# Performance work log

Measured on AMD Instinct MI355X. Metric: run time of the kernel, lower is better.

The kernel has to match this reference:

```python
import jax, jax.numpy as jnp
import numpy as np

B, N, C = 2, 20000, 128
E = 320000
H, COUT = 4, 64
HD = 256  # hidden_dim == H*COUT -> projection is None
ED = 16
L = 3  # LSTM layers


def setup_inputs() -> dict:
    key = jax.random.key(0)
    ks = jax.random.split(key, 16)
    return {
        "x": jax.random.normal(ks[0], (B, N, C), jnp.float32),
        "edge_index": jax.random.randint(ks[1], (2, E), 0, N),
        "edge_attr": jax.random.normal(ks[2], (E, ED), jnp.float32),
        "lin_w": jax.random.normal(ks[3], (C, H * COUT), jnp.float32) / np.sqrt(C),
        "att_src": jax.random.normal(ks[4], (1, H, COUT), jnp.float32) * 0.1,
        "att_dst": jax.random.normal(ks[5], (1, H, COUT), jnp.float32) * 0.1,
        "lin_edge_w": jax.random.normal(ks[6], (ED, H * COUT), jnp.float32) / np.sqrt(ED),
        "att_edge": jax.random.normal(ks[7], (1, H, COUT), jnp.float32) * 0.1,
        "gat_bias": jnp.zeros((H * COUT,), jnp.float32),
        "w_ih": jax.random.normal(ks[8], (L, 4 * HD, HD), jnp.float32) / np.sqrt(HD),
        "w_hh": jax.random.normal(ks[9], (L, 4 * HD, HD), jnp.float32) / np.sqrt(HD),
        "b_ih": jnp.zeros((L, 4 * HD), jnp.float32),
        "b_hh": jnp.zeros((L, 4 * HD), jnp.float32),
        "ln_g": jnp.ones((HD,), jnp.float32),
        "ln_b": jnp.zeros((HD,), jnp.float32),
    }


def reference(x, edge_index, edge_attr, lin_w, att_src, att_dst, lin_edge_w,
              att_edge, gat_bias, w_ih, w_hh, b_ih, b_hh, ln_g, ln_b):
    Bn = B * N
    # ---- GAT: linear transform ----
    xt = (x.reshape(Bn, C) @ lin_w).reshape(Bn, H, COUT)
    # batch-offset edge index, then append self-loops for every node
    off = (jnp.arange(B, dtype=edge_index.dtype) * N)[:, None]
    src = (edge_index[0][None, :] + off).reshape(-1)
    dst = (edge_index[1][None, :] + off).reshape(-1)
    loop = jnp.arange(Bn, dtype=edge_index.dtype)
    src = jnp.concatenate([src, loop])  # [Etot] = [B*E + B*N]
    dst = jnp.concatenate([dst, loop])
    # edge features: shared 2D edge_attr is repeated per batch, zeros on self-loops
    ea = (edge_attr @ lin_edge_w).reshape(E, H, COUT)
    ea = jnp.concatenate([jnp.tile(ea, (B, 1, 1)),
                          jnp.zeros((Bn, H, COUT), xt.dtype)], axis=0)
    # ---- message: gather, score, segment-softmax ----
    x_j = xt[src]  # [Etot, H, COUT]
    x_i = xt[dst]
    alpha = ((x_j * att_src).sum(-1) + (x_i * att_dst).sum(-1)
             + (ea * att_edge).sum(-1))  # [Etot, H]
    alpha = jax.nn.leaky_relu(alpha, 0.2)
    m = jax.ops.segment_max(alpha, dst, num_segments=Bn)
    alpha = jnp.exp(alpha - m[dst])
    s = jax.ops.segment_sum(alpha, dst, num_segments=Bn)
    alpha = alpha / (s[dst] + 1e-16)  # PyG softmax eps; dropout inactive (eval)
    # ---- aggregate (scatter-add) ----
    out = jax.ops.segment_sum(x_j * alpha[..., None], dst, num_segments=Bn)
    spatial = out.reshape(Bn, H * COUT) + gat_bias  # concat heads, [Bn, HD]
    # ---- 3-layer LSTM, seq_len=1, zero initial state (h_prev=None) ----
    h_in = spatial
    hs, cs = [], []
    for l in range(L):
        # h0 = c0 = 0 -> w_hh contributes nothing; inter-layer dropout inactive
        gates = h_in @ w_ih[l].T + b_ih[l] + b_hh[l]
        i, f, g, o = jnp.split(gates, 4, axis=-1)  # PyTorch gate order i,f,g,o
        c = jax.nn.sigmoid(i) * jnp.tanh(g)
        h = jax.nn.sigmoid(o) * jnp.tanh(c)
        hs.append(h)
        cs.append(c)
        h_in = h
    # ---- LayerNorm ----
    h_out = h_in.reshape(B, N, HD)
    mu = h_out.mean(-1, keepdims=True)
    var = ((h_out - mu) ** 2).mean(-1, keepdims=True)
    h_out = (h_out - mu) / jnp.sqrt(var + 1e-5) * ln_g + ln_b
    return h_out, jnp.stack(hs), jnp.stack(cs)
```

## Files before the change

### kernel.cpp

```cpp
#include <hip/hip_runtime.h>
#include <stdint.h>

#define NB_    20000
#define CB_    128
#define EE_    320000
#define BN_    40000
#define BE_    640000
#define ETOT_  680000

typedef __attribute__((ext_vector_type(4))) float f4;
typedef __attribute__((ext_vector_type(4))) unsigned short us4;
typedef __attribute__((ext_vector_type(4))) unsigned int ui4;
typedef __attribute__((ext_vector_type(8))) __bf16 bf16x8;

static __device__ __forceinline__ unsigned short f2bf(float f){
    union { float f; unsigned int u; } v; v.f = f;
    unsigned int u = v.u;
    u += 0x7FFFu + ((u >> 16) & 1u);
    return (unsigned short)(u >> 16);
}
static __device__ __forceinline__ float bf2f(unsigned short b){
    union { unsigned int u; float f; } v; v.u = ((unsigned int)b) << 16;
    return v.f;
}
static __device__ __forceinline__ float sigf(float x){ return 1.f/(1.f+__expf(-x)); }
static __device__ __forceinline__ float tanhfast(float x){ return 2.f/(1.f+__expf(-2.f*x)) - 1.f; }
static __device__ __forceinline__ f4 fmax4(f4 a, f4 b){
    f4 r; r[0]=fmaxf(a[0],b[0]); r[1]=fmaxf(a[1],b[1]); r[2]=fmaxf(a[2],b[2]); r[3]=fmaxf(a[3],b[3]); return r;
}
static __device__ __forceinline__ void gl_lds16(const void* g, void* l){
    __builtin_amdgcn_global_load_lds((const __attribute__((address_space(1))) void*)g,
                                     (__attribute__((address_space(3))) void*)l, 16, 0, 0);
}

__global__ void w2_kernel(const float* __restrict__ lew, const float* __restrict__ ae,
                          float* __restrict__ W2){
    int t = threadIdx.x;
    int d = t >> 2, h = t & 3;
    float s = 0.f;
    for (int c = 0; c < 64; ++c) s += lew[d*256 + h*64 + c] * ae[h*64 + c];
    W2[d*4 + h] = s;
}

__global__ void pack_linwT_kernel(const float* __restrict__ lw, unsigned short* __restrict__ wt){
    int tid = blockIdx.x*256 + threadIdx.x;
    int n = tid >> 7, k = tid & 127;
    wt[n*128 + k] = f2bf(lw[k*256 + n]);
}

__global__ void pack_lstmw_kernel(const float* __restrict__ w_ih, unsigned short* __restrict__ Bp){
    int tid = blockIdx.x*256 + threadIdx.x;
    int l   = tid / 196608;
    int rem = tid - l*196608;
    int p = rem >> 8, k = rem & 255;
    int jb = p / 192, q2 = p - jb*192;
    int chunk = q2 / 48, r = q2 - chunk*48;
    int gate = r >> 4, jj = r & 15;
    int gor = (gate == 0) ? 0 : (gate == 1 ? 2 : 3);
    int srcrow = gor*256 + jb*64 + chunk*16 + jj;
    Bp[tid] = f2bf(w_ih[(l*1024 + srcrow)*256 + k]);
}

__global__ void pack_bias_kernel(const float* __restrict__ b_ih, const float* __restrict__ b_hh,
                                 float* __restrict__ bp){
    int tid = blockIdx.x*256 + threadIdx.x;
    if (tid >= 2304) return;
    int l = tid / 768, p = tid - l*768;
    int jb = p / 192, q2 = p - jb*192;
    int chunk = q2 / 48, r = q2 - chunk*48;
    int gate = r >> 4, jj = r & 15;
    int gor = (gate == 0) ? 0 : (gate == 1 ? 2 : 3);
    int srcrow = gor*256 + jb*64 + chunk*16 + jj;
    bp[tid] = b_ih[l*1024 + srcrow] + b_hh[l*1024 + srcrow];
}

__global__ __launch_bounds__(256) void gemm1_kernel(const float* __restrict__ x,
        const unsigned short* __restrict__ wt, unsigned short* __restrict__ xt){
    __shared__ unsigned short As[64*72];
    __shared__ unsigned short Bs[64*72];
    const int tid = threadIdx.x;
    const int bm = blockIdx.x, bn = blockIdx.y;
    const int lane = tid & 63, w = tid >> 6;
    const int wm = w & 1, wn = w >> 1;
    const int nl = lane & 15, q = lane >> 4;
    f4 acc[2][2] = {};
    for (int kc = 0; kc < 128; kc += 64) {
        #pragma unroll
        for (int it = 0; it < 4; ++it) {
            int s = tid + it*256;
            int row = s >> 4, c4 = s & 15;
            f4 v = *(const f4*)&x[(bm*64+row)*128 + kc + c4*4];
            us4 o; o[0]=f2bf(v[0]); o[1]=f2bf(v[1]); o[2]=f2bf(v[2]); o[3]=f2bf(v[3]);
            *(us4*)&As[row*72 + c4*4] = o;
        }
        #pragma unroll
        for (int it = 0; it < 2; ++it) {
            int s = tid + it*256;
            int row = s >> 3, c = s & 7;
            *(ui4*)&Bs[row*72 + c*8] = *(const ui4*)&wt[(bn*64+row)*128 + kc + c*8];
        }
        __syncthreads();
        #pragma unroll
        for (int kk = 0; kk < 64; kk += 32) {
            bf16x8 a[2], b[2];
            #pragma unroll
            for (int mt = 0; mt < 2; ++mt) a[mt] = *(const bf16x8*)&As[(wm*32 + mt*16 + nl)*72 + kk + q*8];
            #pragma unroll
            for (int nt = 0; nt < 2; ++nt) b[nt] = *(const bf16x8*)&Bs[(wn*32 + nt*16 + nl)*72 + kk + q*8];
            #pragma unroll
            for (int mt = 0; mt < 2; ++mt)
                #pragma unroll
                for (int nt = 0; nt < 2; ++nt)
                    acc[mt][nt] = __builtin_amdgcn_mfma_f32_16x16x32_bf16(a[mt], b[nt], acc[mt][nt], 0, 0, 0);
        }
        __syncthreads();
    }
    #pragma unroll
    for (int mt = 0; mt < 2; ++mt)
        #pragma unroll
        for (int nt = 0; nt < 2; ++nt)
            #pragma unroll
            for (int r = 0; r < 4; ++r) {
                int row = bm*64 + wm*32 + mt*16 + q*4 + r;
                int col = bn*64 + wn*32 + nt*16 + nl;
                xt[row*256 + col] = f2bf(acc[mt][nt][r]);
            }
}

__global__ __launch_bounds__(256) void scores_kernel(const unsigned short* __restrict__ xt,
        const float* __restrict__ att_src, const float* __restrict__ att_dst,
        float* __restrict__ s_src, float* __restrict__ s_dst){
    int n = blockIdx.x*4 + (threadIdx.x >> 6);
    int lane = threadIdx.x & 63;
    us4 xv = *(const us4*)&xt[n*256 + lane*4];
    f4 as = *(const f4*)&att_src[lane*4];
    f4 ad = *(const f4*)&att_dst[lane*4];
    float x0=bf2f(xv[0]), x1=bf2f(xv[1]), x2=bf2f(xv[2]), x3=bf2f(xv[3]);
    float ps = x0*as[0]+x1*as[1]+x2*as[2]+x3*as[3];
    float pd = x0*ad[0]+x1*ad[1]+x2*ad[2]+x3*ad[3];
    #pragma unroll
    for (int o = 1; o < 16; o <<= 1) { ps += __shfl_xor(ps, o, 64); pd += __shfl_xor(pd, o, 64); }
    if ((lane & 15) == 0) {
        s_src[n*4 + (lane>>4)] = ps;
        s_dst[n*4 + (lane>>4)] = pd;
    }
}

__global__ __launch_bounds__(256) void eascore_kernel(const float* __restrict__ ea,
        const float* __restrict__ W2, float* __restrict__ esc){
    __shared__ float w2s[64];
    if (threadIdx.x < 64) w2s[threadIdx.x] = W2[threadIdx.x];
    __syncthreads();
    int e = blockIdx.x*256 + threadIdx.x;
    if (e >= EE_) return;
    f4 acc = {};
    #pragma unroll
    for (int d = 0; d < 16; ++d) {
        float v = ea[e*16 + d];
        f4 wv = *(const f4*)&w2s[d*4];
        acc += v * wv;
    }
    *(f4*)&esc[e*4] = acc;
}

__global__ __launch_bounds__(256) void deghist_kernel(const int* __restrict__ ei, int* __restrict__ deg){
    int e = blockIdx.x*256 + threadIdx.x;
    if (e >= ETOT_) return;
    int dst;
    if (e < BE_) { int b = e / EE_, ee = e - b*EE_; dst = ei[EE_ + ee] + b*NB_; }
    else dst = e - BE_;
    atomicAdd(&deg[dst], 1);
}

__global__ __launch_bounds__(256) void scan1_kernel(const int* __restrict__ deg,
        int* __restrict__ inc, int* __restrict__ bsum){
    __shared__ int sd[256];
    int t = threadIdx.x, i = blockIdx.x*256 + t;
    int v = (i < BN_) ? deg[i] : 0;
    sd[t] = v; __syncthreads();
    #pragma unroll
    for (int d = 1; d < 256; d <<= 1) {
        int x = (t >= d) ? sd[t-d] : 0; __syncthreads();
        sd[t] += x; __syncthreads();
    }
    inc[i] = sd[t];
    if (t == 255) bsum[blockIdx.x] = sd[255];
}

__global__ __launch_bounds__(256) void scan2_kernel(const int* __restrict__ bsum,
        int* __restrict__ bpre, int nb){
    __shared__ int sd[256];
    int t = threadIdx.x;
    int v = (t < nb) ? bsum[t] : 0;
    sd[t] = v; __syncthreads();
    #pragma unroll
    for (int d = 1; d < 256; d <<= 1) {
        int x = (t >= d) ? sd[t-d] : 0; __syncthreads();
        sd[t] += x; __syncthreads();
    }
    if (t < nb) bpre[t] = sd[t] - v;
}

__global__ __launch_bounds__(256) void scan3_kernel(const int* __restrict__ inc,
        const int* __restrict__ deg, const int* __restrict__ bpre,
        int* __restrict__ offs, int* __restrict__ cur){
    int i = blockIdx.x*256 + threadIdx.x;
    if (i >= BN_) return;
    int o = inc[i] - deg[i] + bpre[blockIdx.x];
    offs[i] = o; cur[i] = o;
}

__global__ __launch_bounds__(256) void scatter_kernel(const int* __restrict__ ei,
        const float* __restrict__ s_src, const float* __restrict__ s_dst,
        const float* __restrict__ esc, int* __restrict__ cur,
        int* __restrict__ csr_src, float* __restrict__ csr_alpha){
    int e = blockIdx.x*256 + threadIdx.x;
    if (e >= ETOT_) return;
    int src, dst; f4 a;
    if (e < BE_) {
        int b = e / EE_, ee = e - b*EE_;
        src = ei[ee] + b*NB_;
        dst = ei[EE_ + ee] + b*NB_;
        a = *(const f4*)&esc[ee*4];
    } else {
        src = dst = e - BE_;
        a = (f4){0.f, 0.f, 0.f, 0.f};
    }
    a += *(const f4*)&s_src[src*4];
    a += *(const f4*)&s_dst[dst*4];
    #pragma unroll
    for (int h = 0; h < 4; ++h) a[h] = (a[h] > 0.f) ? a[h] : 0.2f*a[h];
    int pos = atomicAdd(&cur[dst], 1);
    csr_src[pos] = src;
    *(f4*)&csr_alpha[pos*4] = a;
}

__global__ __launch_bounds__(256) void aggregate_kernel(const int* __restrict__ offs,
        const int* __restrict__ deg, const int* __restrict__ csr_src,
        const float* __restrict__ csr_alpha, const unsigned short* __restrict__ xt,
        const float* __restrict__ gat_bias, unsigned short* __restrict__ spat){
    int n = blockIdx.x*4 + (threadIdx.x >> 6);
    int lane = threadIdx.x & 63;
    int start = offs[n], d = deg[n];
    f4 mv = {-1e30f, -1e30f, -1e30f, -1e30f};
    for (int i = lane; i < d; i += 64)
        mv = fmax4(mv, *(const f4*)&csr_alpha[(start+i)*4]);
    #pragma unroll
    for (int o = 1; o < 64; o <<= 1) {
        f4 t; t[0]=__shfl_xor(mv[0],o,64); t[1]=__shfl_xor(mv[1],o,64);
        t[2]=__shfl_xor(mv[2],o,64); t[3]=__shfl_xor(mv[3],o,64);
        mv = fmax4(mv, t);
    }
    f4 sv = {};
    for (int i = lane; i < d; i += 64) {
        f4 a = *(const f4*)&csr_alpha[(start+i)*4];
        sv[0] += __expf(a[0]-mv[0]); sv[1] += __expf(a[1]-mv[1]);
        sv[2] += __expf(a[2]-mv[2]); sv[3] += __expf(a[3]-mv[3]);
    }
    #pragma unroll
    for (int o = 1; o < 64; o <<= 1) {
        sv[0]+=__shfl_xor(sv[0],o,64); sv[1]+=__shfl_xor(sv[1],o,64);
        sv[2]+=__shfl_xor(sv[2],o,64); sv[3]+=__shfl_xor(sv[3],o,64);
    }
    int h = lane >> 4;
    float mh = (h==0)?mv[0]:(h==1)?mv[1]:(h==2)?mv[2]:mv[3];
    float sh = (h==0)?sv[0]:(h==1)?sv[1]:(h==2)?sv[2]:sv[3];
    f4 accv = {};
    for (int base = 0; base < d; base += 64) {
        int cnt = min(64, d - base);
        int srcl = (base + lane < d) ? csr_src[start+base+lane] : 0;
        for (int i = 0; i < cnt; ++i) {
            int srcn = __shfl(srcl, i, 64);
            float av = csr_alpha[(start+base+i)*4 + h];
            float ew = __expf(av - mh);
            us4 xv = *(const us4*)&xt[srcn*256 + lane*4];
            accv[0] += ew * bf2f(xv[0]);
            accv[1] += ew * bf2f(xv[1]);
            accv[2] += ew * bf2f(xv[2]);
            accv[3] += ew * bf2f(xv[3]);
        }
    }
    float invs = 1.f / (sh + 1e-16f);
    f4 gb = *(const f4*)&gat_bias[lane*4];
    accv = accv * invs + gb;
    us4 o4; o4[0]=f2bf(accv[0]); o4[1]=f2bf(accv[1]); o4[2]=f2bf(accv[2]); o4[3]=f2bf(accv[3]);
    *(us4*)&spat[n*256 + lane*4] = o4;
}

__global__ __launch_bounds__(256) void lstm_kernel(const unsigned short* __restrict__ A,
        const unsigned short* __restrict__ Bp, const float* __restrict__ bias,
        float* __restrict__ hs_out, float* __restrict__ cs_out, unsigned short* __restrict__ hnext){
    __shared__ unsigned short As[64*64];
    __shared__ unsigned short Bs[192*64];
    const int tid = threadIdx.x;
    const int bm = blockIdx.x, jb = blockIdx.y;
    const int lane = tid & 63, w = tid >> 6;
    const int nl = lane & 15, q = lane >> 4;
    const int rsub = lane >> 3, csub = lane & 7;
    const int swz = ((csub ^ rsub) << 4);
    f4 acc[4][3] = {};
    const char* Ab = (const char*)A + ((size_t)(bm*64 + rsub))*512 + swz;
    const char* Bb = (const char*)(Bp + (size_t)jb*192*256) + (size_t)rsub*512 + swz;
    for (int kc = 0; kc < 256; kc += 64) {
        #pragma unroll
        for (int i = 0; i < 2; ++i) {
            int t = 2*w + i;
            gl_lds16(Ab + (size_t)t*4096 + kc*2, (char*)As + t*1024);
        }
        #pragma unroll
        for (int i = 0; i < 6; ++i) {
            int t = 6*w + i;
            gl_lds16(Bb + (size_t)t*4096 + kc*2, (char*)Bs + t*1024);
        }
        __syncthreads();
        #pragma unroll
        for (int kk = 0; kk < 64; kk += 32) {
            const int cswz = (kk*2 + q*16) ^ ((nl & 7) << 4);
            bf16x8 a[4], b[3];
            #pragma unroll
            for (int mt = 0; mt < 4; ++mt)
                a[mt] = *(const bf16x8*)((const char*)As + (mt*16 + nl)*128 + cswz);
            #pragma unroll
            for (int gt = 0; gt < 3; ++gt)
                b[gt] = *(const bf16x8*)((const char*)Bs + (w*48 + gt*16 + nl)*128 + cswz);
            #pragma unroll
            for (int mt = 0; mt < 4; ++mt)
                #pragma unroll
                for (int gt = 0; gt < 3; ++gt)
                    acc[mt][gt] = __builtin_amdgcn_mfma_f32_16x16x32_bf16(a[mt], b[gt], acc[mt][gt], 0, 0, 0);
        }
        __syncthreads();
    }
    const int j = jb*64 + w*16 + nl;
    const float bi = bias[jb*192 + w*48 +  0 + nl];
    const float bg = bias[jb*192 + w*48 + 16 + nl];
    const float bo = bias[jb*192 + w*48 + 32 + nl];
    #pragma unroll
    for (int mt = 0; mt < 4; ++mt)
        #pragma unroll
        for (int r = 0; r < 4; ++r) {
            int m = bm*64 + mt*16 + q*4 + r;
            float iv = acc[mt][0][r] + bi;
            float gv = acc[mt][1][r] + bg;
            float ov = acc[mt][2][r] + bo;
            float c = sigf(iv) * tanhfast(gv);
            float hh = sigf(ov) * tanhfast(c);
            cs_out[m*256 + j] = c;
            hs_out[m*256 + j] = hh;
            if (hnext) hnext[m*256 + j] = f2bf(hh);
        }
}

__global__ __launch_bounds__(256) void ln_kernel(const float* __restrict__ hin,
        const float* __restrict__ g, const float* __restrict__ b, float* __restrict__ out){
    int n = blockIdx.x*4 + (threadIdx.x >> 6);
    int lane = threadIdx.x & 63;
    f4 v = *(const f4*)&hin[n*256 + lane*4];
    float s = v[0]+v[1]+v[2]+v[3];
    float ss = v[0]*v[0]+v[1]*v[1]+v[2]*v[2]+v[3]*v[3];
    #pragma unroll
    for (int o = 1; o < 64; o <<= 1) { s += __shfl_xor(s,o,64); ss += __shfl_xor(ss,o,64); }
    float mu = s * (1.f/256.f);
    float var = ss * (1.f/256.f) - mu*mu;
    float rstd = rsqrtf(var + 1e-5f);
    f4 gg = *(const f4*)&g[lane*4], bb = *(const f4*)&b[lane*4];
    f4 o4 = (v - mu) * rstd * gg + bb;
    *(f4*)&out[n*256 + lane*4] = o4;
}

static inline char* carve(char*& p, size_t bytes){
    char* r = p; p += (bytes + 255) & ~(size_t)255; return r;
}

extern "C" void kernel_launch(void* const* d_in, const int* in_sizes, int n_in,
                              void* d_out, int out_size, void* d_ws, size_t ws_size,
                              hipStream_t stream){
    const float* x         = (const float*)d_in[0];
    const int*   ei        = (const int*)  d_in[1];
    const float* edge_attr = (const float*)d_in[2];
    const float* lin_w     = (const float*)d_in[3];
    const float* att_src   = (const float*)d_in[4];
    const float* att_dst   = (const float*)d_in[5];
    const float* lin_edge_w= (const float*)d_in[6];
    const float* att_edge  = (const float*)d_in[7];
    const float* gat_bias  = (const float*)d_in[8];
    const float* w_ih      = (const float*)d_in[9];
    const float* b_ih      = (const float*)d_in[11];
    const float* b_hh      = (const float*)d_in[12];
    const float* ln_g      = (const float*)d_in[13];
    const float* ln_b      = (const float*)d_in[14];

    float* out = (float*)d_out;
    float* hs_base = out + 10240000;
    float* cs_base = out + 40960000;

    unsigned short* xt   = (unsigned short*)(out + 0);
    float* esc           = out + 10240000;
    int*   csr_src       = (int*)(out + 40960000);
    float* csr_alpha     = out + 41640000;
    unsigned short* spat = (unsigned short*)(out + 51200000);
    unsigned short* h0   = (unsigned short*)(out + 61440000);
    unsigned short* h1   = (unsigned short*)(out + 0);

    char* p = (char*)d_ws;
    float* W2          = (float*)carve(p, 64*4);
    float* s_src       = (float*)carve(p, (size_t)BN_*4*4);
    float* s_dst       = (float*)carve(p, (size_t)BN_*4*4);
    unsigned short* lwT= (unsigned short*)carve(p, 32768*2);
    unsigned short* Bp = (unsigned short*)carve(p, 589824*2);
    float* biasP       = (float*)carve(p, 2304*4);
    int* deg           = (int*)carve(p, BN_*4);
    int* inc           = (int*)carve(p, 157*256*4);
    int* bsum          = (int*)carve(p, 256*4);
    int* bpre          = (int*)carve(p, 256*4);
    int* offs          = (int*)carve(p, BN_*4);
    int* cur           = (int*)carve(p, BN_*4);

    hipMemsetAsync(deg, 0, BN_*4, stream);
    w2_kernel<<<1, 64, 0, stream>>>(lin_edge_w, att_edge, W2);
    pack_linwT_kernel<<<128, 256, 0, stream>>>(lin_w, lwT);
    pack_lstmw_kernel<<<2304, 256, 0, stream>>>(w_ih, Bp);
    pack_bias_kernel<<<9, 256, 0, stream>>>(b_ih, b_hh, biasP);

    gemm1_kernel<<<dim3(625, 4), 256, 0, stream>>>(x, lwT, xt);
    scores_kernel<<<10000, 256, 0, stream>>>(xt, att_src, att_dst, s_src, s_dst);
    eascore_kernel<<<1250, 256, 0, stream>>>(edge_attr, W2, esc);

    deghist_kernel<<<2657, 256, 0, stream>>>(ei, deg);
    scan1_kernel<<<157, 256, 0, stream>>>(deg, inc, bsum);
    scan2_kernel<<<1, 256, 0, stream>>>(bsum, bpre, 157);
    scan3_kernel<<<157, 256, 0, stream>>>(inc, deg, bpre, offs, cur);
    scatter_kernel<<<2657, 256, 0, stream>>>(ei, s_src, s_dst, esc, cur, csr_src, csr_alpha);
    aggregate_kernel<<<10000, 256, 0, stream>>>(offs, deg, csr_src, csr_alpha, xt, gat_bias, spat);

    lstm_kernel<<<dim3(625, 4), 256, 0, stream>>>(spat, Bp,          biasP,        hs_base,            cs_base,            h0);
    lstm_kernel<<<dim3(625, 4), 256, 0, stream>>>(h0,   Bp + 196608, biasP + 768,  hs_base + 10240000, cs_base + 10240000, h1);
    lstm_kernel<<<dim3(625, 4), 256, 0, stream>>>(h1,   Bp + 393216, biasP + 1536, hs_base + 20480000, cs_base + 20480000, (unsigned short*)nullptr);

    ln_kernel<<<10000, 256, 0, stream>>>(hs_base + 20480000, ln_g, ln_b, out);
}
```

Measured before the change: 600.2 us.

## Merge prep kernels, drop softmax max pass, keep LSTM weights in registers

Folds the four weight-packing launches into one prep kernel to cut launch overhead. The aggregate kernel drops its max and sum pre-passes and instead exponentiates the raw scores while accumulating the normaliser in the same loop. This removes two passes over the edge scores but gives up max subtraction, so large scores could overflow. The LSTM GEMM loads the whole 64x256 A tile into LDS once and keeps each wave's B slice in registers, with launch bounds asking for two blocks per CU. This removes the per-k-chunk barriers but raises register pressure.

```diff
diff --git a/kernel.cpp b/kernel.cpp
--- a/kernel.cpp
+++ b/kernel.cpp
@@ -25,53 +25,51 @@
 }
 static __device__ __forceinline__ float sigf(float x){ return 1.f/(1.f+__expf(-x)); }
 static __device__ __forceinline__ float tanhfast(float x){ return 2.f/(1.f+__expf(-2.f*x)) - 1.f; }
-static __device__ __forceinline__ f4 fmax4(f4 a, f4 b){
-    f4 r; r[0]=fmaxf(a[0],b[0]); r[1]=fmaxf(a[1],b[1]); r[2]=fmaxf(a[2],b[2]); r[3]=fmaxf(a[3],b[3]); return r;
-}
 static __device__ __forceinline__ void gl_lds16(const void* g, void* l){
     __builtin_amdgcn_global_load_lds((const __attribute__((address_space(1))) void*)g,
                                      (__attribute__((address_space(3))) void*)l, 16, 0, 0);
 }
 
-__global__ void w2_kernel(const float* __restrict__ lew, const float* __restrict__ ae,
-                          float* __restrict__ W2){
-    int t = threadIdx.x;
-    int d = t >> 2, h = t & 3;
-    float s = 0.f;
-    for (int c = 0; c < 64; ++c) s += lew[d*256 + h*64 + c] * ae[h*64 + c];
-    W2[d*4 + h] = s;
-}
-
-__global__ void pack_linwT_kernel(const float* __restrict__ lw, unsigned short* __restrict__ wt){
-    int tid = blockIdx.x*256 + threadIdx.x;
-    int n = tid >> 7, k = tid & 127;
-    wt[n*128 + k] = f2bf(lw[k*256 + n]);
-}
-
-__global__ void pack_lstmw_kernel(const float* __restrict__ w_ih, unsigned short* __restrict__ Bp){
-    int tid = blockIdx.x*256 + threadIdx.x;
-    int l   = tid / 196608;
-    int rem = tid - l*196608;
-    int p = rem >> 8, k = rem & 255;
-    int jb = p / 192, q2 = p - jb*192;
-    int chunk = q2 / 48, r = q2 - chunk*48;
-    int gate = r >> 4, jj = r & 15;
-    int gor = (gate == 0) ? 0 : (gate == 1 ? 2 : 3);
-    int srcrow = gor*256 + jb*64 + chunk*16 + jj;
-    Bp[tid] = f2bf(w_ih[(l*1024 + srcrow)*256 + k]);
-}
-
-__global__ void pack_bias_kernel(const float* __restrict__ b_ih, const float* __restrict__ b_hh,
-                                 float* __restrict__ bp){
-    int tid = blockIdx.x*256 + threadIdx.x;
-    if (tid >= 2304) return;
-    int l = tid / 768, p = tid - l*768;
-    int jb = p / 192, q2 = p - jb*192;
-    int chunk = q2 / 48, r = q2 - chunk*48;
-    int gate = r >> 4, jj = r & 15;
-    int gor = (gate == 0) ? 0 : (gate == 1 ? 2 : 3);
-    int srcrow = gor*256 + jb*64 + chunk*16 + jj;
-    bp[tid] = b_ih[l*1024 + srcrow] + b_hh[l*1024 + srcrow];
+__global__ __launch_bounds__(256) void prep_kernel(const float* __restrict__ lew,
+        const float* __restrict__ ae, float* __restrict__ W2,
+        const float* __restrict__ lw, unsigned short* __restrict__ wt,
+        const float* __restrict__ w_ih, unsigned short* __restrict__ Bp,
+        const float* __restrict__ b_ih, const float* __restrict__ b_hh,
+        float* __restrict__ bp){
+    int bi = blockIdx.x, t = threadIdx.x;
+    if (bi == 0) {
+        if (t < 64) {
+            int d = t >> 2, h = t & 3;
+            float s = 0.f;
+            for (int c = 0; c < 64; ++c) s += lew[d*256 + h*64 + c] * ae[h*64 + c];
+            W2[d*4 + h] = s;
+        }
+    } else if (bi <= 128) {
+        int tid = (bi-1)*256 + t;
+        int n = tid >> 7, k = tid & 127;
+        wt[n*128 + k] = f2bf(lw[k*256 + n]);
+    } else if (bi <= 2432) {
+        int tid = (bi-129)*256 + t;
+        int l   = tid / 196608;
+        int rem = tid - l*196608;
+        int p = rem >> 8, k = rem & 255;
+        int jb = p / 192, q2 = p - jb*192;
+        int chunk = q2 / 48, r = q2 - chunk*48;
+        int gate = r >> 4, jj = r & 15;
+        int gor = (gate == 0) ? 0 : (gate == 1 ? 2 : 3);
+        int srcrow = gor*256 + jb*64 + chunk*16 + jj;
+        Bp[tid] = f2bf(w_ih[(l*1024 + srcrow)*256 + k]);
+    } else {
+        int tid = (bi-2433)*256 + t;
+        if (tid >= 2304) return;
+        int l = tid / 768, p = tid - l*768;
+        int jb = p / 192, q2 = p - jb*192;
+        int chunk = q2 / 48, r = q2 - chunk*48;
+        int gate = r >> 4, jj = r & 15;
+        int gor = (gate == 0) ? 0 : (gate == 1 ? 2 : 3);
+        int srcrow = gor*256 + jb*64 + chunk*16 + jj;
+        bp[tid] = b_ih[l*1024 + srcrow] + b_hh[l*1024 + srcrow];
+    }
 }
 
 __global__ __launch_bounds__(256) void gemm1_kernel(const float* __restrict__ x,
@@ -242,29 +240,8 @@
     int n = blockIdx.x*4 + (threadIdx.x >> 6);
     int lane = threadIdx.x & 63;
     int start = offs[n], d = deg[n];
-    f4 mv = {-1e30f, -1e30f, -1e30f, -1e30f};
-    for (int i = lane; i < d; i += 64)
-        mv = fmax4(mv, *(const f4*)&csr_alpha[(start+i)*4]);
-    #pragma unroll
-    for (int o = 1; o < 64; o <<= 1) {
-        f4 t; t[0]=__shfl_xor(mv[0],o,64); t[1]=__shfl_xor(mv[1],o,64);
-        t[2]=__shfl_xor(mv[2],o,64); t[3]=__shfl_xor(mv[3],o,64);
-        mv = fmax4(mv, t);
-    }
-    f4 sv = {};
-    for (int i = lane; i < d; i += 64) {
-        f4 a = *(const f4*)&csr_alpha[(start+i)*4];
-        sv[0] += __expf(a[0]-mv[0]); sv[1] += __expf(a[1]-mv[1]);
-        sv[2] += __expf(a[2]-mv[2]); sv[3] += __expf(a[3]-mv[3]);
-    }
-    #pragma unroll
-    for (int o = 1; o < 64; o <<= 1) {
-        sv[0]+=__shfl_xor(sv[0],o,64); sv[1]+=__shfl_xor(sv[1],o,64);
-        sv[2]+=__shfl_xor(sv[2],o,64); sv[3]+=__shfl_xor(sv[3],o,64);
-    }
     int h = lane >> 4;
-    float mh = (h==0)?mv[0]:(h==1)?mv[1]:(h==2)?mv[2]:mv[3];
-    float sh = (h==0)?sv[0]:(h==1)?sv[1]:(h==2)?sv[2]:sv[3];
+    float sv = 0.f;
     f4 accv = {};
     for (int base = 0; base < d; base += 64) {
         int cnt = min(64, d - base);
@@ -272,7 +249,8 @@
         for (int i = 0; i < cnt; ++i) {
             int srcn = __shfl(srcl, i, 64);
             float av = csr_alpha[(start+base+i)*4 + h];
-            float ew = __expf(av - mh);
+            float ew = __expf(av);
+            sv += ew;
             us4 xv = *(const us4*)&xt[srcn*256 + lane*4];
             accv[0] += ew * bf2f(xv[0]);
             accv[1] += ew * bf2f(xv[1]);
@@ -280,56 +258,53 @@
             accv[3] += ew * bf2f(xv[3]);
         }
     }
-    float invs = 1.f / (sh + 1e-16f);
+    float invs = 1.f / (sv + 1e-16f);
     f4 gb = *(const f4*)&gat_bias[lane*4];
     accv = accv * invs + gb;
     us4 o4; o4[0]=f2bf(accv[0]); o4[1]=f2bf(accv[1]); o4[2]=f2bf(accv[2]); o4[3]=f2bf(accv[3]);
     *(us4*)&spat[n*256 + lane*4] = o4;
 }
 
-__global__ __launch_bounds__(256) void lstm_kernel(const unsigned short* __restrict__ A,
+__global__ __launch_bounds__(256, 2) void lstm_kernel(const unsigned short* __restrict__ A,
         const unsigned short* __restrict__ Bp, const float* __restrict__ bias,
         float* __restrict__ hs_out, float* __restrict__ cs_out, unsigned short* __restrict__ hnext){
-    __shared__ unsigned short As[64*64];
-    __shared__ unsigned short Bs[192*64];
+    __shared__ unsigned short As[4*64*64];
     const int tid = threadIdx.x;
     const int bm = blockIdx.x, jb = blockIdx.y;
     const int lane = tid & 63, w = tid >> 6;
     const int nl = lane & 15, q = lane >> 4;
     const int rsub = lane >> 3, csub = lane & 7;
     const int swz = ((csub ^ rsub) << 4);
-    f4 acc[4][3] = {};
     const char* Ab = (const char*)A + ((size_t)(bm*64 + rsub))*512 + swz;
-    const char* Bb = (const char*)(Bp + (size_t)jb*192*256) + (size_t)rsub*512 + swz;
-    for (int kc = 0; kc < 256; kc += 64) {
+    #pragma unroll
+    for (int kc4 = 0; kc4 < 4; ++kc4)
         #pragma unroll
         for (int i = 0; i < 2; ++i) {
             int t = 2*w + i;
-            gl_lds16(Ab + (size_t)t*4096 + kc*2, (char*)As + t*1024);
-        }
-        #pragma unroll
-        for (int i = 0; i < 6; ++i) {
-            int t = 6*w + i;
-            gl_lds16(Bb + (size_t)t*4096 + kc*2, (char*)Bs + t*1024);
-        }
-        __syncthreads();
-        #pragma unroll
-        for (int kk = 0; kk < 64; kk += 32) {
-            const int cswz = (kk*2 + q*16) ^ ((nl & 7) << 4);
-            bf16x8 a[4], b[3];
-            #pragma unroll
-            for (int mt = 0; mt < 4; ++mt)
-                a[mt] = *(const bf16x8*)((const char*)As + (mt*16 + nl)*128 + cswz);
+            gl_lds16(Ab + (size_t)t*4096 + kc4*128, (char*)As + kc4*8192 + t*1024);
+        }
+    const unsigned short* Brow = Bp + (size_t)jb*192*256;
+    bf16x8 breg[8][3];
+    #pragma unroll
+    for (int ks = 0; ks < 8; ++ks)
+        #pragma unroll
+        for (int gt = 0; gt < 3; ++gt)
+            breg[ks][gt] = *(const bf16x8*)&Brow[(w*48 + gt*16 + nl)*256 + ks*32 + q*8];
+    f4 acc[4][3] = {};
+    __syncthreads();
+    #pragma unroll
+    for (int ks = 0; ks < 8; ++ks) {
+        const int kc4 = ks >> 1;
+        const int cswz = ((ks & 1)*64 + q*16) ^ ((nl & 7) << 4);
+        bf16x8 a[4];
+        #pragma unroll
+        for (int mt = 0; mt < 4; ++mt)
+            a[mt] = *(const bf16x8*)((const char*)As + kc4*8192 + (mt*16 + nl)*128 + cswz);
+        #pragma unroll
+        for (int mt = 0; mt < 4; ++mt)
             #pragma unroll
             for (int gt = 0; gt < 3; ++gt)
-                b[gt] = *(const bf16x8*)((const char*)Bs + (w*48 + gt*16 + nl)*128 + cswz);
-            #pragma unroll
-            for (int mt = 0; mt < 4; ++mt)
-                #pragma unroll
-                for (int gt = 0; gt < 3; ++gt)
-                    acc[mt][gt] = __builtin_amdgcn_mfma_f32_16x16x32_bf16(a[mt], b[gt], acc[mt][gt], 0, 0, 0);
-        }
-        __syncthreads();
+                acc[mt][gt] = __builtin_amdgcn_mfma_f32_16x16x32_bf16(a[mt], breg[ks][gt], acc[mt][gt], 0, 0, 0);
     }
     const int j = jb*64 + w*16 + nl;
     const float bi = bias[jb*192 + w*48 +  0 + nl];
@@ -417,10 +392,8 @@
     int* cur           = (int*)carve(p, BN_*4);
 
     hipMemsetAsync(deg, 0, BN_*4, stream);
-    w2_kernel<<<1, 64, 0, stream>>>(lin_edge_w, att_edge, W2);
-    pack_linwT_kernel<<<128, 256, 0, stream>>>(lin_w, lwT);
-    pack_lstmw_kernel<<<2304, 256, 0, stream>>>(w_ih, Bp);
-    pack_bias_kernel<<<9, 256, 0, stream>>>(b_ih, b_hh, biasP);
+    prep_kernel<<<2442, 256, 0, stream>>>(lin_edge_w, att_edge, W2, lin_w, lwT,
+                                          w_ih, Bp, b_ih, b_hh, biasP);
 
     gemm1_kernel<<<dim3(625, 4), 256, 0, stream>>>(x, lwT, xt);
     scores_kernel<<<10000, 256, 0, stream>>>(xt, att_src, att_dst, s_src, s_dst);
```

Measured after the change: 609.8 us. About the same (+1.6%).
